# Kernel tuning notes

Hardware: AMD Instinct MI355X
Metric: run time of the kernel (lower is better)

## Reference

```python
import jax, jax.numpy as jnp
import numpy as np


def _lem(x):
    # LEM with mix_margin=1: the depthwise 3x3 'conv' mask has exactly one
    # nonzero per channel, so it's a per-channel circular 1-pixel shift.
    # Channel index mod 5 determines direction:
    #   c%5==0: mask at (m, 2m) -> out(i,j)=x(i, j+1)  -> roll -1 along W
    #   c%5==1: mask at (m, 0)  -> out(i,j)=x(i, j-1)  -> roll +1 along W
    #   c%5==2: mask at (2m, m) -> out(i,j)=x(i+1, j)  -> roll -1 along H
    #   c%5==3: mask at (0, m)  -> out(i,j)=x(i-1, j)  -> roll +1 along H
    #   c%5==4: identity
    B, C, H, W = x.shape
    xr = x.reshape(B, C // 5, 5, H, W)
    out = jnp.stack([
        jnp.roll(xr[:, :, 0], -1, axis=-1),
        jnp.roll(xr[:, :, 1], 1, axis=-1),
        jnp.roll(xr[:, :, 2], -1, axis=-2),
        jnp.roll(xr[:, :, 3], 1, axis=-2),
        xr[:, :, 4],
    ], axis=2)
    return out.reshape(B, C, H, W)


def setup_inputs() -> dict:
    key = jax.random.key(0)
    x = jax.random.normal(key, (8, 320, 128, 128), dtype=jnp.float32)
    return {"x": x}


def reference(x):
    # Ablock spatial paradigm:
    # f = SiLU(lem0(x)); fatt = lem1(sigmoid(f) - 0.5); out = (f + x) * fatt
    f = jax.nn.silu(_lem(x))
    fatt = _lem(jax.nn.sigmoid(f) - 0.5)
    return (f + x) * fatt
```

## Files before the change

kernel.cpp:

```cpp
#include <hip/hip_runtime.h>


#define PLANE_ELEMS 16384

__device__ __forceinline__ float fsig(float z) {
    return __builtin_amdgcn_rcpf(1.0f + __expf(-z));
}

__global__ __launch_bounds__(512) void ablock_kernel(const float* __restrict__ x,
                                                     float* __restrict__ out,
                                                     int nv4) {
    __shared__ float4 s_lds[18][32];
    __shared__ float4 g_lds[18][32];

    int bid = blockIdx.x;
    {
        int nb = gridDim.x;
        if ((nb & 7) == 0) {
            int cpx = nb >> 3;
            bid = (bid & 7) * cpx + (bid >> 3);
        }
    }

    const int tid   = threadIdx.x;
    const int g     = bid * 512 + tid;
    const int lane  = tid & 63;
    const int plane = g >> 12;
    const int o     = g & 4095;
    const int li    = tid >> 5;
    const int c4    = tid & 31;
    const int row   = o >> 5;
    const int t     = plane % 5;

    const float4* p4 = (const float4*)(x + (size_t)plane * PLANE_ELEMS);
    const float4  x0 = p4[o];

    const bool hpath = (t == 2) || (t == 3);
    float4 xh;
    int hidx = 0;
    if (hpath && tid < 64) {
        int k    = tid >> 5;
        int hc4  = tid & 31;
        int row0 = row - li;
        int hrow;
        if (t == 2) { hidx = 16 + k; hrow = (row0 + 16 + k) & 127; }
        else        { hidx = k;      hrow = (row0 - 2 + k) & 127; }
        xh = p4[(hrow << 5) + hc4];
    }

    float4 s, gg;
    s.x = x0.x * fsig(x0.x);  s.y = x0.y * fsig(x0.y);
    s.z = x0.z * fsig(x0.z);  s.w = x0.w * fsig(x0.w);
    gg.x = fsig(s.x) - 0.5f;  gg.y = fsig(s.y) - 0.5f;
    gg.z = fsig(s.z) - 0.5f;  gg.w = fsig(s.w) - 0.5f;

    float4 r;

    if (t == 0) {
        int src = (lane & 32) | ((lane + 1) & 31);
        float snx = __shfl(s.x,  src, 64);
        float gnx = __shfl(gg.x, src, 64);
        float gny = __shfl(gg.y, src, 64);
        r.x = (s.y + x0.x) * gg.z;
        r.y = (s.z + x0.y) * gg.w;
        r.z = (s.w + x0.z) * gnx;
        r.w = (snx + x0.w) * gny;
    } else if (t == 1) {
        int src = (lane & 32) | ((lane - 1) & 31);
        float spw = __shfl(s.w,  src, 64);
        float gpz = __shfl(gg.z, src, 64);
        float gpw = __shfl(gg.w, src, 64);
        r.x = (spw + x0.x) * gpz;
        r.y = (s.x + x0.y) * gpw;
        r.z = (s.y + x0.z) * gg.x;
        r.w = (s.z + x0.w) * gg.y;
    } else if (t == 4) {
        r.x = (s.x + x0.x) * gg.x;
        r.y = (s.y + x0.y) * gg.y;
        r.z = (s.z + x0.z) * gg.z;
        r.w = (s.w + x0.w) * gg.w;
    } else {
        const int base = (t == 2) ? li : li + 2;
        s_lds[base][c4] = s;
        g_lds[base][c4] = gg;

        if (tid < 64) {
            int hc4 = tid & 31;
            float4 hs, hg;
            hs.x = xh.x * fsig(xh.x);  hs.y = xh.y * fsig(xh.y);
            hs.z = xh.z * fsig(xh.z);  hs.w = xh.w * fsig(xh.w);
            hg.x = fsig(hs.x) - 0.5f;  hg.y = fsig(hs.y) - 0.5f;
            hg.z = fsig(hs.z) - 0.5f;  hg.w = fsig(hs.w) - 0.5f;
            s_lds[hidx][hc4] = hs;
            g_lds[hidx][hc4] = hg;
        }
        __syncthreads();

        float4 s1 = s_lds[li + 1][c4];
        float4 g2;
        if (t == 2) g2 = g_lds[li + 2][c4];
        else        g2 = g_lds[li][c4];
        r.x = (s1.x + x0.x) * g2.x;
        r.y = (s1.y + x0.y) * g2.y;
        r.z = (s1.z + x0.z) * g2.z;
        r.w = (s1.w + x0.w) * g2.w;
    }

    ((float4*)out)[g] = r;
}

extern "C" void kernel_launch(void* const* d_in, const int* in_sizes, int n_in,
                              void* d_out, int out_size, void* d_ws, size_t ws_size,
                              hipStream_t stream) {
    const float* x   = (const float*)d_in[0];
    float*       out = (float*)d_out;
    int n   = in_sizes[0];
    int nv4 = n >> 2;
    int block = 512;
    int grid  = nv4 / block;
    ablock_kernel<<<grid, block, 0, stream>>>(x, out, nv4);
}
```

Baseline: 273.9 us.

## Process two 16-row tiles per block to halve halo overhead and grid size

Each 512-thread block now covers 32 rows of a plane instead of 16, with each thread loading and computing two float4 values (rows li and li+16). This halves the number of blocks and the redundant halo-row loads and sigmoid recomputation for the H-shift channels, and gives more memory-level parallelism per thread. The XCD-aware block index swizzle is removed, and LDS per block doubles.

```diff
diff --git a/kernel.cpp b/kernel.cpp
--- a/kernel.cpp
+++ b/kernel.cpp
@@ -10,79 +10,75 @@
 __global__ __launch_bounds__(512) void ablock_kernel(const float* __restrict__ x,
                                                      float* __restrict__ out,
                                                      int nv4) {
-    __shared__ float4 s_lds[18][32];
-    __shared__ float4 g_lds[18][32];
-
-    int bid = blockIdx.x;
-    {
-        int nb = gridDim.x;
-        if ((nb & 7) == 0) {
-            int cpx = nb >> 3;
-            bid = (bid & 7) * cpx + (bid >> 3);
-        }
-    }
+    __shared__ float4 s_lds[34][32];
+    __shared__ float4 g_lds[34][32];
 
     const int tid   = threadIdx.x;
-    const int g     = bid * 512 + tid;
     const int lane  = tid & 63;
-    const int plane = g >> 12;
-    const int o     = g & 4095;
     const int li    = tid >> 5;
     const int c4    = tid & 31;
-    const int row   = o >> 5;
+    const int plane = blockIdx.x >> 2;
+    const int row0  = (blockIdx.x & 3) << 5;
     const int t     = plane % 5;
 
     const float4* p4 = (const float4*)(x + (size_t)plane * PLANE_ELEMS);
-    const float4  x0 = p4[o];
+    const int oA = ((row0 + li) << 5) + c4;
+    const int oB = ((row0 + li + 16) << 5) + c4;
+
+    const float4 xA = p4[oA];
+    const float4 xB = p4[oB];
 
     const bool hpath = (t == 2) || (t == 3);
     float4 xh;
     int hidx = 0;
     if (hpath && tid < 64) {
-        int k    = tid >> 5;
-        int hc4  = tid & 31;
-        int row0 = row - li;
+        int k   = tid >> 5;
+        int hc4 = tid & 31;
         int hrow;
-        if (t == 2) { hidx = 16 + k; hrow = (row0 + 16 + k) & 127; }
+        if (t == 2) { hidx = 32 + k; hrow = (row0 + 32 + k) & 127; }
         else        { hidx = k;      hrow = (row0 - 2 + k) & 127; }
         xh = p4[(hrow << 5) + hc4];
     }
 
-    float4 s, gg;
-    s.x = x0.x * fsig(x0.x);  s.y = x0.y * fsig(x0.y);
-    s.z = x0.z * fsig(x0.z);  s.w = x0.w * fsig(x0.w);
-    gg.x = fsig(s.x) - 0.5f;  gg.y = fsig(s.y) - 0.5f;
-    gg.z = fsig(s.z) - 0.5f;  gg.w = fsig(s.w) - 0.5f;
+    float4 sA, gA, sB, gB;
+    sA.x = xA.x * fsig(xA.x);  sB.x = xB.x * fsig(xB.x);
+    sA.y = xA.y * fsig(xA.y);  sB.y = xB.y * fsig(xB.y);
+    sA.z = xA.z * fsig(xA.z);  sB.z = xB.z * fsig(xB.z);
+    sA.w = xA.w * fsig(xA.w);  sB.w = xB.w * fsig(xB.w);
+    gA.x = fsig(sA.x) - 0.5f;  gB.x = fsig(sB.x) - 0.5f;
+    gA.y = fsig(sA.y) - 0.5f;  gB.y = fsig(sB.y) - 0.5f;
+    gA.z = fsig(sA.z) - 0.5f;  gB.z = fsig(sB.z) - 0.5f;
+    gA.w = fsig(sA.w) - 0.5f;  gB.w = fsig(sB.w) - 0.5f;
 
-    float4 r;
+    float4 rA, rB;
 
     if (t == 0) {
         int src = (lane & 32) | ((lane + 1) & 31);
-        float snx = __shfl(s.x,  src, 64);
-        float gnx = __shfl(gg.x, src, 64);
-        float gny = __shfl(gg.y, src, 64);
-        r.x = (s.y + x0.x) * gg.z;
-        r.y = (s.z + x0.y) * gg.w;
-        r.z = (s.w + x0.z) * gnx;
-        r.w = (snx + x0.w) * gny;
+        float snxA = __shfl(sA.x, src, 64), snxB = __shfl(sB.x, src, 64);
+        float gnxA = __shfl(gA.x, src, 64), gnxB = __shfl(gB.x, src, 64);
+        float gnyA = __shfl(gA.y, src, 64), gnyB = __shfl(gB.y, src, 64);
+        rA.x = (sA.y + xA.x) * gA.z;   rB.x = (sB.y + xB.x) * gB.z;
+        rA.y = (sA.z + xA.y) * gA.w;   rB.y = (sB.z + xB.y) * gB.w;
+        rA.z = (sA.w + xA.z) * gnxA;   rB.z = (sB.w + xB.z) * gnxB;
+        rA.w = (snxA + xA.w) * gnyA;   rB.w = (snxB + xB.w) * gnyB;
     } else if (t == 1) {
         int src = (lane & 32) | ((lane - 1) & 31);
-        float spw = __shfl(s.w,  src, 64);
-        float gpz = __shfl(gg.z, src, 64);
-        float gpw = __shfl(gg.w, src, 64);
-        r.x = (spw + x0.x) * gpz;
-        r.y = (s.x + x0.y) * gpw;
-        r.z = (s.y + x0.z) * gg.x;
-        r.w = (s.z + x0.w) * gg.y;
+        float spwA = __shfl(sA.w, src, 64), spwB = __shfl(sB.w, src, 64);
+        float gpzA = __shfl(gA.z, src, 64), gpzB = __shfl(gB.z, src, 64);
+        float gpwA = __shfl(gA.w, src, 64), gpwB = __shfl(gB.w, src, 64);
+        rA.x = (spwA + xA.x) * gpzA;   rB.x = (spwB + xB.x) * gpzB;
+        rA.y = (sA.x + xA.y) * gpwA;   rB.y = (sB.x + xB.y) * gpwB;
+        rA.z = (sA.y + xA.z) * gA.x;   rB.z = (sB.y + xB.z) * gB.x;
+        rA.w = (sA.z + xA.w) * gA.y;   rB.w = (sB.z + xB.w) * gB.y;
     } else if (t == 4) {
-        r.x = (s.x + x0.x) * gg.x;
-        r.y = (s.y + x0.y) * gg.y;
-        r.z = (s.z + x0.z) * gg.z;
-        r.w = (s.w + x0.w) * gg.w;
+        rA.x = (sA.x + xA.x) * gA.x;   rB.x = (sB.x + xB.x) * gB.x;
+        rA.y = (sA.y + xA.y) * gA.y;   rB.y = (sB.y + xB.y) * gB.y;
+        rA.z = (sA.z + xA.z) * gA.z;   rB.z = (sB.z + xB.z) * gB.z;
+        rA.w = (sA.w + xA.w) * gA.w;   rB.w = (sB.w + xB.w) * gB.w;
     } else {
         const int base = (t == 2) ? li : li + 2;
-        s_lds[base][c4] = s;
-        g_lds[base][c4] = gg;
+        s_lds[base][c4]      = sA;  g_lds[base][c4]      = gA;
+        s_lds[base + 16][c4] = sB;  g_lds[base + 16][c4] = gB;
 
         if (tid < 64) {
             int hc4 = tid & 31;
@@ -96,17 +92,20 @@
         }
         __syncthreads();
 
-        float4 s1 = s_lds[li + 1][c4];
-        float4 g2;
-        if (t == 2) g2 = g_lds[li + 2][c4];
-        else        g2 = g_lds[li][c4];
-        r.x = (s1.x + x0.x) * g2.x;
-        r.y = (s1.y + x0.y) * g2.y;
-        r.z = (s1.z + x0.z) * g2.z;
-        r.w = (s1.w + x0.w) * g2.w;
+        float4 s1A = s_lds[li + 1][c4];
+        float4 s1B = s_lds[li + 17][c4];
+        float4 g2A, g2B;
+        if (t == 2) { g2A = g_lds[li + 2][c4];  g2B = g_lds[li + 18][c4]; }
+        else        { g2A = g_lds[li][c4];      g2B = g_lds[li + 16][c4]; }
+        rA.x = (s1A.x + xA.x) * g2A.x;   rB.x = (s1B.x + xB.x) * g2B.x;
+        rA.y = (s1A.y + xA.y) * g2A.y;   rB.y = (s1B.y + xB.y) * g2B.y;
+        rA.z = (s1A.z + xA.z) * g2A.z;   rB.z = (s1B.z + xB.z) * g2B.z;
+        rA.w = (s1A.w + xA.w) * g2A.w;   rB.w = (s1B.w + xB.w) * g2B.w;
     }
 
-    ((float4*)out)[g] = r;
+    float4* o4 = (float4*)out + (size_t)plane * 4096;
+    o4[oA] = rA;
+    o4[oB] = rB;
 }
 
 extern "C" void kernel_launch(void* const* d_in, const int* in_sizes, int n_in,
@@ -117,6 +116,6 @@
     int n   = in_sizes[0];
     int nv4 = n >> 2;
     int block = 512;
-    int grid  = nv4 / block;
+    int grid  = nv4 / (block * 2);
     ablock_kernel<<<grid, block, 0, stream>>>(x, out, nv4);
 }
```

New measurement: 277.3 us. No clear change (+1.2%).
